# Kernel tuning notes

Hardware: AMD Instinct MI355X
Metric: run time of the kernel (lower is better)

The kernel has to match this reference:

```python
import jax, jax.numpy as jnp
import numpy as np

EPS = 1e-6
B, N, I, H, O, L = 8, 2048, 64, 128, 8, 3
K = O * L
ITERS, TAU, LAM, KNN = 3, 0.1, 0.5, 5

def _ln(x, g, b):
    m = x.mean(-1, keepdims=True)
    v = jnp.mean((x - m) ** 2, -1, keepdims=True)
    return (x - m) / jnp.sqrt(v + 1e-5) * g + b

def _gelu(x):
    return jax.nn.gelu(x, approximate=False)


def setup_inputs():
    ks = jax.random.split(jax.random.key(0), 16)
    rn = lambda k, sh, s=0.05: jax.random.normal(k, sh, jnp.float32) * s
    return {
        'x': jax.random.normal(ks[0], (B, N, I), jnp.float32),
        'enc_w1': rn(ks[1], (H, I)), 'enc_b1': jnp.zeros((H,), jnp.float32),
        'enc_g1': jnp.ones((H,), jnp.float32), 'enc_bb1': jnp.zeros((H,), jnp.float32),
        'enc_w2': rn(ks[2], (H, H)), 'enc_b2': jnp.zeros((H,), jnp.float32),
        'enc_g2': jnp.ones((H,), jnp.float32), 'enc_bb2': jnp.zeros((H,), jnp.float32),
        'sp_w1': rn(ks[3], (H, H + 1)), 'sp_b1': jnp.zeros((H,), jnp.float32),
        'sp_g': jnp.ones((H,), jnp.float32), 'sp_bb': jnp.zeros((H,), jnp.float32),
        'sp_w2': rn(ks[4], (1, H), 0.005), 'sp_b2': jnp.zeros((1,), jnp.float32),
        'object_space': rn(ks[5], (1, O, H), 0.1),
        'horizon_scale': jnp.float32(0.3),
        'level_times': jnp.array([1.0, 2.5, 4.0], jnp.float32),
        'base_horizons': jnp.array([0.9, 0.6, 0.3], jnp.float32),
        'gru_w_ih': rn(ks[6], (3 * H, H)), 'gru_w_hh': rn(ks[7], (3 * H, H)),
        'gru_b_ih': jnp.zeros((3 * H,), jnp.float32), 'gru_b_hh': jnp.zeros((3 * H,), jnp.float32),
        'mlp_w1': rn(ks[8], (H, H)), 'mlp_b1': jnp.zeros((H,), jnp.float32),
        'mlp_w2': rn(ks[9], (H, H)), 'mlp_b2': jnp.zeros((H,), jnp.float32),
        'norm_g': jnp.ones((H,), jnp.float32), 'norm_b': jnp.zeros((H,), jnp.float32),
    }


def reference(x, enc_w1, enc_b1, enc_g1, enc_bb1, enc_w2, enc_b2, enc_g2, enc_bb2, sp_w1, sp_b1, sp_g, sp_bb, sp_w2, sp_b2, object_space, horizon_scale, level_times, base_horizons, gru_w_ih, gru_w_hh, gru_b_ih, gru_b_hh, mlp_w1, mlp_b1, mlp_w2, mlp_b2, norm_g, norm_b):
    # feature encoder: Linear -> LN -> GELU -> Linear -> LN
    h = _gelu(_ln(x @ enc_w1.T + enc_b1, enc_g1, enc_bb1))
    spatial = _ln(h @ enc_w2.T + enc_b2, enc_g2, enc_bb2)  # (B,N,H)
    # local density via kNN mean distance (torch.cdist equivalent)
    sq = jnp.sum(x * x, -1)
    d2 = sq[:, :, None] + sq[:, None, :] - 2.0 * jnp.einsum('bnd,bmd->bnm', x, x)
    dist = jnp.sqrt(jnp.maximum(d2, 0.0))
    knn = -jax.lax.top_k(-dist, KNN + 1)[0]           # k+1 smallest, ascending
    density = jnp.tanh(knn[..., 1:].mean(-1))          # (B,N)
    # scale predictor: Linear -> LN -> GELU -> Linear -> Softplus
    s = jnp.concatenate([spatial, density[..., None]], -1)
    s = _gelu(_ln(s @ sp_w1.T + sp_b1, sp_g, sp_bb))
    pred_scale = jax.nn.softplus(s @ sp_w2.T + sp_b2)  # (B,N,1)
    pred_time = 5.0 - 1.5 * density[..., None] + 0.5 * pred_scale
    features = jnp.concatenate([pred_time, spatial], -1)  # (B,N,H+1)
    # scale-adaptive horizons, tiled object-major to match slot layout
    hz = jnp.clip(base_horizons[None, :, None] + (horizon_scale * (density - 0.5))[:, None, :], 0.1, 1.0)
    horizons = jnp.tile(hz, (1, O, 1))                 # (B,K,N)
    # worldlines
    obj = jnp.broadcast_to(object_space, (B, O, H))
    times = jnp.broadcast_to(jnp.tile(level_times, O)[None, :, None], (B, K, 1))
    slots = jnp.concatenate([times, jnp.repeat(obj, L, axis=1)], -1)  # (B,K,H+1)
    feats_sp = features[..., 1:]
    old_flat = obj.reshape(-1, H)
    attn = None
    for _ in range(ITERS):
        diff = features[:, None, :, :] - slots[:, :, None, :]  # (B,K,N,H+1)
        dt = diff[..., 0]
        dr2 = jnp.sum(diff[..., 1:] ** 2, -1)
        ls = dt * dt - dr2
        d_L = jnp.sign(ls) * jnp.sqrt(jnp.abs(ls) + EPS)
        r = jnp.sqrt(dr2)
        cone = horizons - r / (jnp.abs(dt) + EPS) - 10.0 * jax.nn.relu(-dt) - 5.0 * jax.nn.relu(r - jnp.abs(dt))
        logits = -jnp.abs(d_L) + LAM * jnp.tanh(cone)
        attn = jax.nn.softmax(logits / TAU, axis=1)      # softmax over slots
        w = attn / (attn.sum(2, keepdims=True) + 1e-8)
        upd = jnp.einsum('bkn,bnh->bkh', w, feats_sp)
        obj_upd = upd.reshape(B, O, L, H).sum(2).reshape(-1, H)
        # GRUCell (torch semantics)
        gi = obj_upd @ gru_w_ih.T + gru_b_ih
        gh = old_flat @ gru_w_hh.T + gru_b_hh
        gi_r, gi_z, gi_n = jnp.split(gi, 3, -1)
        gh_r, gh_z, gh_n = jnp.split(gh, 3, -1)
        rg = jax.nn.sigmoid(gi_r + gh_r)
        zg = jax.nn.sigmoid(gi_z + gh_z)
        ng = jnp.tanh(gi_n + rg * gh_n)
        new = ((1.0 - zg) * ng + zg * old_flat).reshape(B, O, H)
        t = _gelu(_ln(new, norm_g, norm_b) @ mlp_w1.T + mlp_b1) @ mlp_w2.T + mlp_b2
        new = new + 0.2 * t
        slots = jnp.concatenate([times, jnp.repeat(new, L, axis=1)], -1)
    return slots, attn, pred_time[..., 0], density
```

## Files before the change

kernel.cpp:

```cpp
#include <hip/hip_runtime.h>
#include <math.h>

constexpr int cB = 8, cN = 2048, cI = 64, cH = 128, cO = 8, cK = 24;
constexpr int ROWS = cB * cN;

constexpr size_t WS_SPATIAL = 0;
constexpr size_t WS_SQ      = WS_SPATIAL + (size_t)ROWS * cH;
constexpr size_t WS_GHS     = WS_SQ + ROWS;
constexpr size_t WS_NSQ0    = WS_GHS + (size_t)cO * 3 * cH;
constexpr size_t WS_NEWOBJ  = WS_NSQ0 + cO;
constexpr size_t WS_NSQ     = WS_NEWOBJ + (size_t)cB * cO * cH;
constexpr size_t WS_W1T     = WS_NSQ + (size_t)cB * cO;
constexpr size_t WS_W2T     = WS_W1T + 8192;
constexpr size_t WS_HW1T    = WS_W2T + 16384;
constexpr size_t WS_UPD3    = WS_HW1T + 16896;
constexpr size_t WS_S3      = WS_UPD3 + (size_t)3 * cB * cK * cH;
constexpr size_t WS_XBF     = WS_S3 + (size_t)3 * cB * cK;

constexpr size_t OUT_SLOTS = 0;
constexpr size_t OUT_ATTN  = (size_t)cB * cK * 129;
constexpr size_t OUT_PT    = OUT_ATTN + (size_t)cB * cK * cN;
constexpr size_t OUT_DEN   = OUT_PT + (size_t)cB * cN;

typedef __attribute__((ext_vector_type(8))) short bf16x8;
typedef __attribute__((ext_vector_type(4))) float f32x4;

__device__ __forceinline__ float gelu_f(float v){
  return 0.5f * v * (1.f + erff(v * 0.70710678118654752440f));
}
__device__ __forceinline__ short f2bf(float f){
  unsigned u = __float_as_uint(f);
  u += 0x7fffu + ((u >> 16) & 1u);
  return (short)(u >> 16);
}
__device__ __forceinline__ bf16x8 pack8(float4 a, float4 b){
  bf16x8 r;
  r[0]=f2bf(a.x); r[1]=f2bf(a.y); r[2]=f2bf(a.z); r[3]=f2bf(a.w);
  r[4]=f2bf(b.x); r[5]=f2bf(b.y); r[6]=f2bf(b.z); r[7]=f2bf(b.w);
  return r;
}
__device__ __forceinline__ float wred(float a){
  a += __shfl_xor(a, 1); a += __shfl_xor(a, 2); a += __shfl_xor(a, 4);
  a += __shfl_xor(a, 8); a += __shfl_xor(a, 16); a += __shfl_xor(a, 32);
  return a;
}

__global__ __launch_bounds__(256) void k_cvt_sq(const float* __restrict__ x, short* __restrict__ xbf,
                                                float* __restrict__ sq){
  int t = threadIdx.x;
  size_t base = (size_t)blockIdx.x * 2048;
  int r = t >> 3, e0 = (t & 7) * 8;
  const float4* xp = (const float4*)(x + base + (size_t)r * cI + e0);
  float4 v0 = xp[0], v1 = xp[1];
  *(bf16x8*)(xbf + base + (size_t)r * cI + e0) = pack8(v0, v1);
  float s = v0.x*v0.x + v0.y*v0.y + v0.z*v0.z + v0.w*v0.w
          + v1.x*v1.x + v1.y*v1.y + v1.z*v1.z + v1.w*v1.w;
  s += __shfl_xor(s, 1); s += __shfl_xor(s, 2); s += __shfl_xor(s, 4);
  if ((t & 7) == 0) sq[blockIdx.x * 32 + r] = s;
}

__global__ __launch_bounds__(256) void k_prep(const float* __restrict__ objsp, const float* __restrict__ w_hh,
                                              const float* __restrict__ b_hh,
                                              const float* __restrict__ ew1, const float* __restrict__ ew2,
                                              const float* __restrict__ spw1,
                                              float* __restrict__ ghs, float* __restrict__ nsq0,
                                              float* __restrict__ w1t, float* __restrict__ w2t,
                                              float* __restrict__ hw1t){
  int id = blockIdx.x * 256 + threadIdx.x;
  if (id < cO * 3 * cH){
    int o = id / (3 * cH), j = id % (3 * cH);
    const float* wr = w_hh + (size_t)j * cH;
    const float* ob = objsp + (size_t)o * cH;
    float a0=0,a1=0,a2=0,a3=0;
    #pragma unroll
    for (int h = 0; h < cH; h += 4){
      a0 += wr[h]*ob[h]; a1 += wr[h+1]*ob[h+1]; a2 += wr[h+2]*ob[h+2]; a3 += wr[h+3]*ob[h+3];
    }
    ghs[id] = (a0+a1)+(a2+a3) + b_hh[j];
  } else if (id < cO * 3 * cH + cO){
    int o = id - cO * 3 * cH;
    const float* ob = objsp + (size_t)o * cH;
    float s = 0.f;
    for (int h = 0; h < cH; ++h) s += ob[h]*ob[h];
    nsq0[o] = s;
  } else {
    int idx = id - (cO * 3 * cH + cO);
    if (idx < 8192){
      int dc = idx >> 9, rem = idx & 511, f = rem >> 2, j = rem & 3;
      w1t[idx] = ew1[f * cI + dc * 4 + j];
    } else if (idx < 24576){
      int k2 = idx - 8192;
      int dc = k2 >> 9, rem = k2 & 511, f = rem >> 2, j = rem & 3;
      w2t[k2] = ew2[f * cH + dc * 4 + j];
    } else if (idx < 41472){
      int k3 = idx - 24576;
      int dc = k3 >> 9, rem = k3 & 511, f = rem >> 2, j = rem & 3;
      int d = dc * 4 + j;
      hw1t[k3] = (d < 129) ? spw1[f * 129 + d] : 0.f;
    }
  }
}

__global__ __launch_bounds__(256) void k_pairwise(const short* __restrict__ xbf, const float* __restrict__ sq,
                                                  float* __restrict__ den_out){
  __shared__ float cand[4][16][101];
  int b  = blockIdx.x >> 7;
  int rt = blockIdx.x & 127;
  int r0 = rt * 16;
  int lane = threadIdx.x & 63, w = threadIdx.x >> 6;
  const short* xb = xbf + (size_t)b * cN * cI;

  int arow = r0 + (lane & 15);
  int koff = (lane >> 4) * 8;
  const bf16x8* ap = (const bf16x8*)(xb + (size_t)arow * cI + koff);
  bf16x8 a0 = ap[0];
  bf16x8 a1 = ap[4];

  float sqr[4];
  int rg0 = r0 + ((lane >> 4) << 2);
  #pragma unroll
  for (int j = 0; j < 4; ++j) sqr[j] = sq[b * cN + rg0 + j];

  float t6[4][6];
  #pragma unroll
  for (int j = 0; j < 4; ++j){
    #pragma unroll
    for (int q = 0; q < 6; ++q) t6[j][q] = 3e38f;
  }

  int cbase = w * 512;
  #pragma unroll 2
  for (int ct = 0; ct < 32; ++ct){
    int col0 = cbase + ct * 16;
    int brow = col0 + (lane & 15);
    const bf16x8* bp = (const bf16x8*)(xb + (size_t)brow * cI + koff);
    bf16x8 b0 = bp[0];
    bf16x8 b1 = bp[4];
    f32x4 acc = {0.f, 0.f, 0.f, 0.f};
    acc = __builtin_amdgcn_mfma_f32_16x16x32_bf16(a0, b0, acc, 0, 0, 0);
    acc = __builtin_amdgcn_mfma_f32_16x16x32_bf16(a1, b1, acc, 0, 0, 0);
    float sqc = sq[b * cN + col0 + (lane & 15)];
    #pragma unroll
    for (int j = 0; j < 4; ++j){
      float d2 = sqr[j] + sqc - 2.f * acc[j];
      d2 = fmaxf(d2, 0.f);
      if (d2 < t6[j][5]){
        if (d2 < t6[j][4]){ t6[j][5]=t6[j][4];
          if (d2 < t6[j][3]){ t6[j][4]=t6[j][3];
            if (d2 < t6[j][2]){ t6[j][3]=t6[j][2];
              if (d2 < t6[j][1]){ t6[j][2]=t6[j][1];
                if (d2 < t6[j][0]){ t6[j][1]=t6[j][0]; t6[j][0]=d2; } else t6[j][1]=d2;
              } else t6[j][2]=d2;
            } else t6[j][3]=d2;
          } else t6[j][4]=d2;
        } else t6[j][5]=d2;
      }
    }
  }
  int rloc = (lane >> 4) << 2;
  #pragma unroll
  for (int j = 0; j < 4; ++j){
    #pragma unroll
    for (int q = 0; q < 6; ++q) cand[w][rloc + j][(lane & 15) * 6 + q] = t6[j][q];
  }
  __syncthreads();
  int tt = threadIdx.x;
  if (tt < 64){
    int ww = tt >> 4, rr = tt & 15;
    const float* c = cand[ww][rr];
    float m0=3e38f,m1=3e38f,m2=3e38f,m3=3e38f,m4=3e38f,m5=3e38f;
    #pragma unroll
    for (int q = 0; q < 96; ++q){
      float v = c[q];
      if (v < m5){
        if (v<m4){ m5=m4; if (v<m3){ m4=m3; if (v<m2){ m3=m2; if (v<m1){ m2=m1; if (v<m0){ m1=m0; m0=v; } else m1=v; } else m2=v; } else m3=v; } else m4=v; } else m5=v;
      }
    }
    float* cw = cand[ww][rr];
    cw[0]=m0; cw[1]=m1; cw[2]=m2; cw[3]=m3; cw[4]=m4; cw[5]=m5;
  }
  __syncthreads();
  if (tt < 16){
    float m0=3e38f,m1=3e38f,m2=3e38f,m3=3e38f,m4=3e38f,m5=3e38f;
    #pragma unroll
    for (int ww = 0; ww < 4; ++ww){
      const float* c = cand[ww][tt];
      #pragma unroll
      for (int q = 0; q < 6; ++q){
        float v = c[q];
        if (v < m5){
          if (v<m4){ m5=m4; if (v<m3){ m4=m3; if (v<m2){ m3=m2; if (v<m1){ m2=m1; if (v<m0){ m1=m0; m0=v; } else m1=v; } else m2=v; } else m3=v; } else m4=v; } else m5=v;
        }
      }
    }
    float md = (sqrtf(m1)+sqrtf(m2)+sqrtf(m3)+sqrtf(m4)+sqrtf(m5)) * 0.2f;
    den_out[b * cN + r0 + tt] = tanhf(md);
  }
}

__global__ __launch_bounds__(256) void k_enc_head(const float* __restrict__ x, const float* __restrict__ den_in,
    const float* __restrict__ w1t, const float* __restrict__ b1v, const float* __restrict__ g1, const float* __restrict__ bb1,
    const float* __restrict__ w2t, const float* __restrict__ b2v, const float* __restrict__ g2, const float* __restrict__ bb2,
    const float* __restrict__ hw1t, const float* __restrict__ hb1, const float* __restrict__ hg, const float* __restrict__ hbb,
    const float* __restrict__ hw2, const float* __restrict__ hb2,
    float* __restrict__ spatial, float* __restrict__ pt_out){
  __shared__ __align__(16) float xbuf[16][68];
  __shared__ __align__(16) float hbuf[16][132];
  const int t = threadIdx.x, lane = t & 63, wid = t >> 6;
  const int row0 = blockIdx.x * 16;
  const int rbase = wid * 4;
  const int f0 = lane * 2;

  {
    const float4* xs = (const float4*)(x + (size_t)row0 * cI);
    float4 v = xs[t];
    *(float4*)&xbuf[t >> 4][(t & 15) * 4] = v;
  }
  if (t < 16){
    float dn = den_in[row0 + t];
    float* hd = &hbuf[t][128];
    hd[0] = dn; hd[1] = 0.f; hd[2] = 0.f; hd[3] = 0.f;
  }
  __syncthreads();

  float2 b1p  = *(const float2*)(b1v + f0);
  float2 g1p  = *(const float2*)(g1  + f0);
  float2 bb1p = *(const float2*)(bb1 + f0);
  float2 b2p  = *(const float2*)(b2v + f0);
  float2 g2p  = *(const float2*)(g2  + f0);
  float2 bb2p = *(const float2*)(bb2 + f0);
  float2 hb1p = *(const float2*)(hb1 + f0);
  float2 hgp  = *(const float2*)(hg  + f0);
  float2 hbbp = *(const float2*)(hbb + f0);
  float2 hw2p = *(const float2*)(hw2 + f0);

  float accA[4], accB[4];

  #pragma unroll
  for (int r = 0; r < 4; ++r){ accA[r] = b1p.x; accB[r] = b1p.y; }
  #pragma unroll 4
  for (int dc = 0; dc < 16; ++dc){
    float4 wA = *(const float4*)(w1t + ((size_t)dc * cH + f0) * 4);
    float4 wB = *(const float4*)(w1t + ((size_t)dc * cH + f0 + 1) * 4);
    #pragma unroll
    for (int r = 0; r < 4; ++r){
      float4 xv = *(const float4*)&xbuf[rbase + r][dc * 4];
      accA[r] += wA.x*xv.x + wA.y*xv.y + wA.z*xv.z + wA.w*xv.w;
      accB[r] += wB.x*xv.x + wB.y*xv.y + wB.z*xv.z + wB.w*xv.w;
    }
  }
  #pragma unroll
  for (int r = 0; r < 4; ++r){
    float sm = wred(accA[r] + accB[r]);
    float s2 = wred(accA[r]*accA[r] + accB[r]*accB[r]);
    float mean = sm * (1.f/128.f);
    float rstd = rsqrtf(s2 * (1.f/128.f) - mean*mean + 1e-5f);
    float hA = gelu_f((accA[r]-mean)*rstd*g1p.x + bb1p.x);
    float hB = gelu_f((accB[r]-mean)*rstd*g1p.y + bb1p.y);
    float2 hv = { hA, hB };
    *(float2*)&hbuf[rbase + r][f0] = hv;
  }
  __syncthreads();

  #pragma unroll
  for (int r = 0; r < 4; ++r){ accA[r] = b2p.x; accB[r] = b2p.y; }
  #pragma unroll 4
  for (int dc = 0; dc < 32; ++dc){
    float4 wA = *(const float4*)(w2t + ((size_t)dc * cH + f0) * 4);
    float4 wB = *(const float4*)(w2t + ((size_t)dc * cH + f0 + 1) * 4);
    #pragma unroll
    for (int r = 0; r < 4; ++r){
      float4 hv = *(const float4*)&hbuf[rbase + r][dc * 4];
      accA[r] += wA.x*hv.x + wA.y*hv.y + wA.z*hv.z + wA.w*hv.w;
      accB[r] += wB.x*hv.x + wB.y*hv.y + wB.z*hv.z + wB.w*hv.w;
    }
  }
  #pragma unroll
  for (int r = 0; r < 4; ++r){
    float sm = wred(accA[r] + accB[r]);
    float s2 = wred(accA[r]*accA[r] + accB[r]*accB[r]);
    float mean = sm * (1.f/128.f);
    float rstd = rsqrtf(s2 * (1.f/128.f) - mean*mean + 1e-5f);
    float sA = (accA[r]-mean)*rstd*g2p.x + bb2p.x;
    float sB = (accB[r]-mean)*rstd*g2p.y + bb2p.y;
    float2 sv = { sA, sB };
    *(float2*)(spatial + (size_t)(row0 + rbase + r) * cH + f0) = sv;
    *(float2*)&hbuf[rbase + r][f0] = sv;
  }
  __syncthreads();

  #pragma unroll
  for (int r = 0; r < 4; ++r){ accA[r] = hb1p.x; accB[r] = hb1p.y; }
  #pragma unroll 4
  for (int dc = 0; dc < 33; ++dc){
    float4 wA = *(const float4*)(hw1t + ((size_t)dc * cH + f0) * 4);
    float4 wB = *(const float4*)(hw1t + ((size_t)dc * cH + f0 + 1) * 4);
    #pragma unroll
    for (int r = 0; r < 4; ++r){
      float4 hv = *(const float4*)&hbuf[rbase + r][dc * 4];
      accA[r] += wA.x*hv.x + wA.y*hv.y + wA.z*hv.z + wA.w*hv.w;
      accB[r] += wB.x*hv.x + wB.y*hv.y + wB.z*hv.z + wB.w*hv.w;
    }
  }
  #pragma unroll
  for (int r = 0; r < 4; ++r){
    float sm = wred(accA[r] + accB[r]);
    float s2 = wred(accA[r]*accA[r] + accB[r]*accB[r]);
    float mean = sm * (1.f/128.f);
    float rstd = rsqrtf(s2 * (1.f/128.f) - mean*mean + 1e-5f);
    float e0 = gelu_f((accA[r]-mean)*rstd*hgp.x + hbbp.x);
    float e1 = gelu_f((accB[r]-mean)*rstd*hgp.y + hbbp.y);
    float part = wred(e0*hw2p.x + e1*hw2p.y);
    if (lane == r){
      float ps = part + hb2[0];
      float spl = fmaxf(ps, 0.f) + log1pf(expf(-fabsf(ps)));
      float dn = hbuf[rbase + r][128];
      pt_out[row0 + rbase + r] = 5.f - 1.5f*dn + 0.5f*spl;
    }
  }
}

__global__ __launch_bounds__(256) void k_attn_upd(const float* __restrict__ spatial, const float* __restrict__ pt_in,
    const float* __restrict__ den_in, const float* __restrict__ objp, int ob_stride,
    const float* __restrict__ nsqp, int nq_stride,
    const float* __restrict__ lt, const float* __restrict__ bh, const float* __restrict__ hs,
    float* __restrict__ attn_out, int writeAttn,
    float* __restrict__ upd_raw, float* __restrict__ Ssum){
  __shared__ float abuf[24][65];
  int blk = blockIdx.x;
  int b = blk >> 5, chunk = blk & 31;
  int n0 = chunk * 64;
  int t = threadIdx.x;
  int sub = t & 3, rl = t >> 2;
  int id = b * cN + n0 + rl;

  {
    float4 sv[8];
    const float4* sp4 = (const float4*)(spatial + (size_t)id * cH + sub * 32);
    #pragma unroll
    for (int i = 0; i < 8; ++i) sv[i] = sp4[i];
    float spn2 = 0.f;
    #pragma unroll
    for (int i = 0; i < 8; ++i) spn2 += sv[i].x*sv[i].x + sv[i].y*sv[i].y + sv[i].z*sv[i].z + sv[i].w*sv[i].w;

    const float* ob = objp + (size_t)b * ob_stride;
    float acc[8];
    #pragma unroll
    for (int o = 0; o < 8; ++o){
      const float4* orow = (const float4*)(ob + (size_t)o * cH + sub * 32);
      float a0=0,a1=0,a2=0,a3=0;
      #pragma unroll
      for (int i = 0; i < 8; ++i){ float4 w4 = orow[i];
        a0 += w4.x*sv[i].x; a1 += w4.y*sv[i].y; a2 += w4.z*sv[i].z; a3 += w4.w*sv[i].w; }
      acc[o] = (a0+a1)+(a2+a3);
    }
    spn2 += __shfl_xor(spn2, 1); spn2 += __shfl_xor(spn2, 2);
    #pragma unroll
    for (int o = 0; o < 8; ++o){ acc[o] += __shfl_xor(acc[o], 1); acc[o] += __shfl_xor(acc[o], 2); }

    if (sub == 0){
      const float* nq = nsqp + (size_t)b * nq_stride;
      float nsqv_[8];
      #pragma unroll
      for (int o = 0; o < 8; ++o) nsqv_[o] = nq[o];
      float pt = pt_in[id], den = den_in[id];
      float hsv = hs[0];
      float lts[3] = { lt[0], lt[1], lt[2] };
      float bhs[3] = { bh[0], bh[1], bh[2] };

      float logits[24];
      #pragma unroll
      for (int k = 0; k < 24; ++k){
        const int o = k / 3, l = k % 3;
        float dtv = pt - lts[l];
        float dr2 = fmaxf(spn2 + nsqv_[o] - 2.f * acc[o], 0.f);
        float ls  = dtv*dtv - dr2;
        float adL = sqrtf(fabsf(ls) + 1e-6f);
        float r   = sqrtf(dr2);
        float adt = fabsf(dtv);
        float hz  = fminf(fmaxf(bhs[l] + hsv * (den - 0.5f), 0.1f), 1.0f);
        float cone = hz - r / (adt + 1e-6f) - 10.f * fmaxf(-dtv, 0.f) - 5.f * fmaxf(r - adt, 0.f);
        logits[k] = (-adL + 0.5f * tanhf(cone)) * 10.f;
      }
      float mx = -3e38f;
      #pragma unroll
      for (int k = 0; k < 24; ++k) mx = fmaxf(mx, logits[k]);
      float es[24]; float ssum = 0.f;
      #pragma unroll
      for (int k = 0; k < 24; ++k){ es[k] = expf(logits[k] - mx); ssum += es[k]; }
      float inv = 1.f / ssum;
      #pragma unroll
      for (int k = 0; k < 24; ++k) abuf[k][rl] = es[k] * inv;
    }
  }
  __syncthreads();

  if (writeAttn){
    float* ao = attn_out + (size_t)b * cK * cN + n0;
    #pragma unroll
    for (int i = 0; i < 6; ++i){
      int idx = t + i * 256;
      ao[(size_t)(idx >> 6) * cN + (idx & 63)] = abuf[idx >> 6][idx & 63];
    }
  }

  int h = t & 127, g = t >> 7;
  float acc2[12];
  #pragma unroll
  for (int kk = 0; kk < 12; ++kk) acc2[kk] = 0.f;
  const float* sp = spatial + ((size_t)b * cN + n0) * cH + h;
  for (int ni = 0; ni < 64; ++ni){
    float spv = sp[(size_t)ni * cH];
    #pragma unroll
    for (int kk = 0; kk < 12; ++kk) acc2[kk] += abuf[g*12+kk][ni] * spv;
  }
  #pragma unroll
  for (int kk = 0; kk < 12; ++kk)
    atomicAdd(&upd_raw[((size_t)b * cK + g*12+kk) * cH + h], acc2[kk]);
  if (t < 24){
    float s = 0.f;
    #pragma unroll
    for (int j = 0; j < 64; ++j) s += abuf[t][j];
    atomicAdd(&Ssum[b * cK + t], s);
  }
}

__global__ __launch_bounds__(128) void k_gru(const float* __restrict__ upd_raw, const float* __restrict__ Ssum,
    const float* __restrict__ ghs, const float* __restrict__ objsp,
    const float* __restrict__ w_ih, const float* __restrict__ b_ih,
    const float* __restrict__ mw1, const float* __restrict__ mb1,
    const float* __restrict__ mw2, const float* __restrict__ mb2,
    const float* __restrict__ ng_, const float* __restrict__ nb_,
    const float* __restrict__ lt,
    float* __restrict__ newobj, float* __restrict__ nsq,
    float* __restrict__ slots_out, int writeSlots){
  __shared__ float ubuf[cH], lbuf[cH], gbuf[cH], red[8];
  int bo = blockIdx.x; int b = bo >> 3, o = bo & 7;
  int t = threadIdx.x;
  int lane = t & 63, wid = t >> 6;

  float u = 0.f;
  #pragma unroll
  for (int l = 0; l < 3; ++l){
    int k = o * 3 + l;
    float s = Ssum[b * cK + k] + 1e-8f;
    u += upd_raw[((size_t)b * cK + k) * cH + t] / s;
  }
  ubuf[t] = u;
  __syncthreads();

  float gi[3];
  #pragma unroll
  for (int j3 = 0; j3 < 3; ++j3){
    const float* wr = w_ih + ((size_t)j3 * cH + t) * cH;
    float a0=0,a1=0,a2=0,a3=0;
    #pragma unroll
    for (int d = 0; d < cH; d += 4){
      a0 += wr[d]*ubuf[d]; a1 += wr[d+1]*ubuf[d+1]; a2 += wr[d+2]*ubuf[d+2]; a3 += wr[d+3]*ubuf[d+3];
    }
    gi[j3] = (a0+a1)+(a2+a3) + b_ih[j3 * cH + t];
  }
  const float* gh = ghs + (size_t)o * 3 * cH;
  float ghr = gh[t], ghz = gh[cH + t], ghn = gh[2 * cH + t];
  float oldv = objsp[(size_t)o * cH + t];
  float rg = 1.f / (1.f + expf(-(gi[0] + ghr)));
  float zg = 1.f / (1.f + expf(-(gi[1] + ghz)));
  float ngv = tanhf(gi[2] + rg * ghn);
  float nv = (1.f - zg) * ngv + zg * oldv;

  float s1 = nv, s2 = nv * nv;
  #pragma unroll
  for (int m = 1; m < 64; m <<= 1){ s1 += __shfl_xor(s1, m); s2 += __shfl_xor(s2, m); }
  if (lane == 0){ red[wid] = s1; red[4 + wid] = s2; }
  __syncthreads();
  float mean = (red[0] + red[1]) * (1.f/128.f);
  float var  = (red[4] + red[5]) * (1.f/128.f) - mean * mean;
  float ln = (nv - mean) * rsqrtf(var + 1e-5f) * ng_[t] + nb_[t];
  lbuf[t] = ln;
  __syncthreads();

  const float* w1r = mw1 + (size_t)t * cH;
  {
    float a0=0,a1=0,a2=0,a3=0;
    #pragma unroll
    for (int d = 0; d < cH; d += 4){
      a0 += w1r[d]*lbuf[d]; a1 += w1r[d+1]*lbuf[d+1]; a2 += w1r[d+2]*lbuf[d+2]; a3 += w1r[d+3]*lbuf[d+3];
    }
    gbuf[t] = gelu_f((a0+a1)+(a2+a3) + mb1[t]);
  }
  __syncthreads();
  const float* w2r = mw2 + (size_t)t * cH;
  float m2v;
  {
    float a0=0,a1=0,a2=0,a3=0;
    #pragma unroll
    for (int d = 0; d < cH; d += 4){
      a0 += w2r[d]*gbuf[d]; a1 += w2r[d+1]*gbuf[d+1]; a2 += w2r[d+2]*gbuf[d+2]; a3 += w2r[d+3]*gbuf[d+3];
    }
    m2v = (a0+a1)+(a2+a3) + mb2[t];
  }
  float outv = nv + 0.2f * m2v;
  newobj[((size_t)b * cO + o) * cH + t] = outv;

  float qv = outv * outv;
  #pragma unroll
  for (int m = 1; m < 64; m <<= 1) qv += __shfl_xor(qv, m);
  __syncthreads();
  if (lane == 0) red[wid] = qv;
  __syncthreads();
  if (t == 0) nsq[b * cO + o] = red[0] + red[1];

  if (writeSlots){
    #pragma unroll
    for (int l = 0; l < 3; ++l){
      size_t base = ((size_t)b * cK + o * 3 + l) * 129;
      slots_out[base + 1 + t] = outv;
      if (t == 0) slots_out[base] = lt[l];
    }
  }
}

extern "C" void kernel_launch(void* const* d_in, const int* in_sizes, int n_in,
                              void* d_out, int out_size, void* d_ws, size_t ws_size,
                              hipStream_t stream){
  const float* x       = (const float*)d_in[0];
  const float* enc_w1  = (const float*)d_in[1];
  const float* enc_b1  = (const float*)d_in[2];
  const float* enc_g1  = (const float*)d_in[3];
  const float* enc_bb1 = (const float*)d_in[4];
  const float* enc_w2  = (const float*)d_in[5];
  const float* enc_b2  = (const float*)d_in[6];
  const float* enc_g2  = (const float*)d_in[7];
  const float* enc_bb2 = (const float*)d_in[8];
  const float* sp_w1   = (const float*)d_in[9];
  const float* sp_b1   = (const float*)d_in[10];
  const float* sp_g    = (const float*)d_in[11];
  const float* sp_bb   = (const float*)d_in[12];
  const float* sp_w2   = (const float*)d_in[13];
  const float* sp_b2   = (const float*)d_in[14];
  const float* objsp   = (const float*)d_in[15];
  const float* hscale  = (const float*)d_in[16];
  const float* ltimes  = (const float*)d_in[17];
  const float* bhor    = (const float*)d_in[18];
  const float* gw_ih   = (const float*)d_in[19];
  const float* gw_hh   = (const float*)d_in[20];
  const float* gb_ih   = (const float*)d_in[21];
  const float* gb_hh   = (const float*)d_in[22];
  const float* mw1     = (const float*)d_in[23];
  const float* mb1     = (const float*)d_in[24];
  const float* mw2     = (const float*)d_in[25];
  const float* mb2     = (const float*)d_in[26];
  const float* normg   = (const float*)d_in[27];
  const float* normb   = (const float*)d_in[28];
  (void)in_sizes; (void)n_in; (void)out_size; (void)ws_size;

  float* out = (float*)d_out;
  float* ws  = (float*)d_ws;

  float* spatial = ws + WS_SPATIAL;
  float* sq      = ws + WS_SQ;
  float* ghs     = ws + WS_GHS;
  float* nsq0    = ws + WS_NSQ0;
  float* newobj  = ws + WS_NEWOBJ;
  float* nsqv    = ws + WS_NSQ;
  float* w1t     = ws + WS_W1T;
  float* w2t     = ws + WS_W2T;
  float* hw1t    = ws + WS_HW1T;
  float* updr3   = ws + WS_UPD3;
  float* Ss3     = ws + WS_S3;
  short* xbf     = (short*)(ws + WS_XBF);

  hipMemsetAsync((void*)updr3, 0, (size_t)(3 * cB * cK * cH + 3 * cB * cK) * sizeof(float), stream);

  k_cvt_sq<<<dim3(ROWS / 32), dim3(256), 0, stream>>>(x, xbf, sq);
  k_prep<<<dim3(175), dim3(256), 0, stream>>>(objsp, gw_hh, gb_hh, enc_w1, enc_w2, sp_w1,
                                              ghs, nsq0, w1t, w2t, hw1t);
  k_pairwise<<<dim3(cB * (cN / 16)), dim3(256), 0, stream>>>(xbf, sq, out + OUT_DEN);
  k_enc_head<<<dim3(ROWS / 16), dim3(256), 0, stream>>>(x, out + OUT_DEN,
      w1t, enc_b1, enc_g1, enc_bb1, w2t, enc_b2, enc_g2, enc_bb2,
      hw1t, sp_b1, sp_g, sp_bb, sp_w2, sp_b2,
      spatial, out + OUT_PT);

  for (int it = 0; it < 3; ++it){
    float* updr = updr3 + (size_t)it * cB * cK * cH;
    float* Ss   = Ss3 + (size_t)it * cB * cK;
    const float* objp = (it == 0) ? objsp : newobj;
    int obst = (it == 0) ? 0 : cO * cH;
    const float* nqp = (it == 0) ? nsq0 : nsqv;
    int nqst = (it == 0) ? 0 : cO;
    k_attn_upd<<<dim3(cB * 32), dim3(256), 0, stream>>>(spatial, out + OUT_PT, out + OUT_DEN,
                                                        objp, obst, nqp, nqst,
                                                        ltimes, bhor, hscale,
                                                        out + OUT_ATTN, (it == 2) ? 1 : 0,
                                                        updr, Ss);
    k_gru<<<dim3(cB * cO), dim3(128), 0, stream>>>(updr, Ss, ghs, objsp, gw_ih, gb_ih,
                                                   mw1, mb1, mw2, mb2, normg, normb, ltimes,
                                                   newobj, nsqv, out + OUT_SLOTS, (it == 2) ? 1 : 0);
  }
}
```

Measured before the change: 340.5 us.

## Move encoder and spatial-head GEMMs to split-bf16 MFMA with pre-fragmented weights

Replaces the scalar FP32 dot-product loops in the encoder and spatial-head kernel with 16x16x32 bf16 MFMA instructions. Activations and weights are each split into hi and lo bf16 parts, and three MFMAs per tile approximate FP32 accuracy. The prep kernel now writes the weights in MFMA fragment order. Each wave handles 16 rows, with XOR-swizzled LDS buffers and per-wave layernorm reductions over 16 lanes. This cuts ALU time in the encoder but adds conversion work and some loss of precision from dropping the lo*lo term.

After: 315.0 us. 7.5% less time.

```diff
diff --git a/kernel.cpp b/kernel.cpp
--- a/kernel.cpp
+++ b/kernel.cpp
@@ -10,12 +10,17 @@
 constexpr size_t WS_NSQ0    = WS_GHS + (size_t)cO * 3 * cH;
 constexpr size_t WS_NEWOBJ  = WS_NSQ0 + cO;
 constexpr size_t WS_NSQ     = WS_NEWOBJ + (size_t)cB * cO * cH;
-constexpr size_t WS_W1T     = WS_NSQ + (size_t)cB * cO;
-constexpr size_t WS_W2T     = WS_W1T + 8192;
-constexpr size_t WS_HW1T    = WS_W2T + 16384;
-constexpr size_t WS_UPD3    = WS_HW1T + 16896;
+constexpr size_t WS_WFRAG   = WS_NSQ + (size_t)cB * cO;
+constexpr size_t WS_UPD3    = WS_WFRAG + 45056;
 constexpr size_t WS_S3      = WS_UPD3 + (size_t)3 * cB * cK * cH;
 constexpr size_t WS_XBF     = WS_S3 + (size_t)3 * cB * cK;
+
+constexpr size_t WF_W1H = 0;
+constexpr size_t WF_W1L = 8192;
+constexpr size_t WF_W2H = 16384;
+constexpr size_t WF_W2L = 32768;
+constexpr size_t WF_WHH = 49152;
+constexpr size_t WF_WHL = 69632;
 
 constexpr size_t OUT_SLOTS = 0;
 constexpr size_t OUT_ATTN  = (size_t)cB * cK * 129;
@@ -32,6 +37,9 @@
   unsigned u = __float_as_uint(f);
   u += 0x7fffu + ((u >> 16) & 1u);
   return (short)(u >> 16);
+}
+__device__ __forceinline__ float bf2f(short h){
+  return __uint_as_float(((unsigned)(unsigned short)h) << 16);
 }
 __device__ __forceinline__ bf16x8 pack8(float4 a, float4 b){
   bf16x8 r;
@@ -39,10 +47,23 @@
   r[4]=f2bf(b.x); r[5]=f2bf(b.y); r[6]=f2bf(b.z); r[7]=f2bf(b.w);
   return r;
 }
-__device__ __forceinline__ float wred(float a){
-  a += __shfl_xor(a, 1); a += __shfl_xor(a, 2); a += __shfl_xor(a, 4);
-  a += __shfl_xor(a, 8); a += __shfl_xor(a, 16); a += __shfl_xor(a, 32);
+__device__ __forceinline__ float qred16(float a){
+  a += __shfl_xor(a, 1); a += __shfl_xor(a, 2); a += __shfl_xor(a, 4); a += __shfl_xor(a, 8);
   return a;
+}
+__device__ __forceinline__ void load_split_frag(const float* buf, int off, bf16x8& hi, bf16x8& lo){
+  float4 u0 = *(const float4*)&buf[off];
+  float4 u1 = *(const float4*)&buf[off + 4];
+  float v[8] = {u0.x,u0.y,u0.z,u0.w,u1.x,u1.y,u1.z,u1.w};
+  #pragma unroll
+  for (int i = 0; i < 8; ++i){
+    short h = f2bf(v[i]);
+    hi[i] = h;
+    lo[i] = f2bf(v[i] - bf2f(h));
+  }
+}
+__device__ __forceinline__ int lidx(int row, int col, int stride){
+  return row * stride + (col ^ ((row & 3) << 3));
 }
 
 __global__ __launch_bounds__(256) void k_cvt_sq(const float* __restrict__ x, short* __restrict__ xbf,
@@ -64,8 +85,7 @@
                                               const float* __restrict__ ew1, const float* __restrict__ ew2,
                                               const float* __restrict__ spw1,
                                               float* __restrict__ ghs, float* __restrict__ nsq0,
-                                              float* __restrict__ w1t, float* __restrict__ w2t,
-                                              float* __restrict__ hw1t){
+                                              short* __restrict__ wf){
   int id = blockIdx.x * 256 + threadIdx.x;
   if (id < cO * 3 * cH){
     int o = id / (3 * cH), j = id % (3 * cH);
@@ -85,19 +105,34 @@
     nsq0[o] = s;
   } else {
     int idx = id - (cO * 3 * cH + cO);
+    if (idx >= 45056) return;
+    float w; size_t hoff, loff;
+    int e, nc;
     if (idx < 8192){
-      int dc = idx >> 9, rem = idx & 511, f = rem >> 2, j = rem & 3;
-      w1t[idx] = ew1[f * cI + dc * 4 + j];
+      e = idx; nc = 2;
+      int i = e & 7, l = (e >> 3) & 63, r = e >> 9;
+      int c = r % nc, ft = r / nc;
+      int f = ft * 16 + (l & 15), k = c * 32 + (l >> 4) * 8 + i;
+      w = ew1[f * cI + k];
+      hoff = WF_W1H + e; loff = WF_W1L + e;
     } else if (idx < 24576){
-      int k2 = idx - 8192;
-      int dc = k2 >> 9, rem = k2 & 511, f = rem >> 2, j = rem & 3;
-      w2t[k2] = ew2[f * cH + dc * 4 + j];
-    } else if (idx < 41472){
-      int k3 = idx - 24576;
-      int dc = k3 >> 9, rem = k3 & 511, f = rem >> 2, j = rem & 3;
-      int d = dc * 4 + j;
-      hw1t[k3] = (d < 129) ? spw1[f * 129 + d] : 0.f;
-    }
+      e = idx - 8192; nc = 4;
+      int i = e & 7, l = (e >> 3) & 63, r = e >> 9;
+      int c = r % nc, ft = r / nc;
+      int f = ft * 16 + (l & 15), k = c * 32 + (l >> 4) * 8 + i;
+      w = ew2[f * cH + k];
+      hoff = WF_W2H + e; loff = WF_W2L + e;
+    } else {
+      e = idx - 24576; nc = 5;
+      int i = e & 7, l = (e >> 3) & 63, r = e >> 9;
+      int c = r % nc, ft = r / nc;
+      int f = ft * 16 + (l & 15), k = c * 32 + (l >> 4) * 8 + i;
+      w = (k < 129) ? spw1[f * 129 + k] : 0.f;
+      hoff = WF_WHH + e; loff = WF_WHL + e;
+    }
+    short h = f2bf(w);
+    wf[hoff] = h;
+    wf[loff] = f2bf(w - bf2f(h));
   }
 }
 
@@ -198,124 +233,197 @@
   }
 }
 
-__global__ __launch_bounds__(256) void k_enc_head(const float* __restrict__ x, const float* __restrict__ den_in,
-    const float* __restrict__ w1t, const float* __restrict__ b1v, const float* __restrict__ g1, const float* __restrict__ bb1,
-    const float* __restrict__ w2t, const float* __restrict__ b2v, const float* __restrict__ g2, const float* __restrict__ bb2,
-    const float* __restrict__ hw1t, const float* __restrict__ hb1, const float* __restrict__ hg, const float* __restrict__ hbb,
+__global__ __launch_bounds__(128) void k_enc_head(const float* __restrict__ x, const float* __restrict__ den_in,
+    const short* __restrict__ wf,
+    const float* __restrict__ b1, const float* __restrict__ g1, const float* __restrict__ bb1,
+    const float* __restrict__ b2, const float* __restrict__ g2, const float* __restrict__ bb2,
+    const float* __restrict__ hb1, const float* __restrict__ hg, const float* __restrict__ hbb,
     const float* __restrict__ hw2, const float* __restrict__ hb2,
     float* __restrict__ spatial, float* __restrict__ pt_out){
-  __shared__ __align__(16) float xbuf[16][68];
-  __shared__ __align__(16) float hbuf[16][132];
-  const int t = threadIdx.x, lane = t & 63, wid = t >> 6;
-  const int row0 = blockIdx.x * 16;
-  const int rbase = wid * 4;
-  const int f0 = lane * 2;
+  __shared__ __align__(16) float xs_[2][16 * 68];
+  __shared__ __align__(16) float hs_[2][16 * 164];
+  const int t = threadIdx.x, lane = t & 63, wv = t >> 6;
+  const int row0 = blockIdx.x * 32 + wv * 16;
+  float* xbuf = xs_[wv];
+  float* hbuf = hs_[wv];
+  const int r15 = lane & 15, q = lane >> 4;
+  const int qx = (q ^ (r15 & 3)) << 3;
 
   {
-    const float4* xs = (const float4*)(x + (size_t)row0 * cI);
-    float4 v = xs[t];
-    *(float4*)&xbuf[t >> 4][(t & 15) * 4] = v;
-  }
-  if (t < 16){
-    float dn = den_in[row0 + t];
-    float* hd = &hbuf[t][128];
-    hd[0] = dn; hd[1] = 0.f; hd[2] = 0.f; hd[3] = 0.f;
-  }
-  __syncthreads();
-
-  float2 b1p  = *(const float2*)(b1v + f0);
-  float2 g1p  = *(const float2*)(g1  + f0);
-  float2 bb1p = *(const float2*)(bb1 + f0);
-  float2 b2p  = *(const float2*)(b2v + f0);
-  float2 g2p  = *(const float2*)(g2  + f0);
-  float2 bb2p = *(const float2*)(bb2 + f0);
-  float2 hb1p = *(const float2*)(hb1 + f0);
-  float2 hgp  = *(const float2*)(hg  + f0);
-  float2 hbbp = *(const float2*)(hbb + f0);
-  float2 hw2p = *(const float2*)(hw2 + f0);
-
-  float accA[4], accB[4];
-
-  #pragma unroll
-  for (int r = 0; r < 4; ++r){ accA[r] = b1p.x; accB[r] = b1p.y; }
-  #pragma unroll 4
-  for (int dc = 0; dc < 16; ++dc){
-    float4 wA = *(const float4*)(w1t + ((size_t)dc * cH + f0) * 4);
-    float4 wB = *(const float4*)(w1t + ((size_t)dc * cH + f0 + 1) * 4);
-    #pragma unroll
-    for (int r = 0; r < 4; ++r){
-      float4 xv = *(const float4*)&xbuf[rbase + r][dc * 4];
-      accA[r] += wA.x*xv.x + wA.y*xv.y + wA.z*xv.z + wA.w*xv.w;
-      accB[r] += wB.x*xv.x + wB.y*xv.y + wB.z*xv.z + wB.w*xv.w;
-    }
-  }
-  #pragma unroll
-  for (int r = 0; r < 4; ++r){
-    float sm = wred(accA[r] + accB[r]);
-    float s2 = wred(accA[r]*accA[r] + accB[r]*accB[r]);
-    float mean = sm * (1.f/128.f);
-    float rstd = rsqrtf(s2 * (1.f/128.f) - mean*mean + 1e-5f);
-    float hA = gelu_f((accA[r]-mean)*rstd*g1p.x + bb1p.x);
-    float hB = gelu_f((accB[r]-mean)*rstd*g1p.y + bb1p.y);
-    float2 hv = { hA, hB };
-    *(float2*)&hbuf[rbase + r][f0] = hv;
-  }
-  __syncthreads();
-
-  #pragma unroll
-  for (int r = 0; r < 4; ++r){ accA[r] = b2p.x; accB[r] = b2p.y; }
-  #pragma unroll 4
-  for (int dc = 0; dc < 32; ++dc){
-    float4 wA = *(const float4*)(w2t + ((size_t)dc * cH + f0) * 4);
-    float4 wB = *(const float4*)(w2t + ((size_t)dc * cH + f0 + 1) * 4);
-    #pragma unroll
-    for (int r = 0; r < 4; ++r){
-      float4 hv = *(const float4*)&hbuf[rbase + r][dc * 4];
-      accA[r] += wA.x*hv.x + wA.y*hv.y + wA.z*hv.z + wA.w*hv.w;
-      accB[r] += wB.x*hv.x + wB.y*hv.y + wB.z*hv.z + wB.w*hv.w;
-    }
-  }
-  #pragma unroll
-  for (int r = 0; r < 4; ++r){
-    float sm = wred(accA[r] + accB[r]);
-    float s2 = wred(accA[r]*accA[r] + accB[r]*accB[r]);
-    float mean = sm * (1.f/128.f);
-    float rstd = rsqrtf(s2 * (1.f/128.f) - mean*mean + 1e-5f);
-    float sA = (accA[r]-mean)*rstd*g2p.x + bb2p.x;
-    float sB = (accB[r]-mean)*rstd*g2p.y + bb2p.y;
-    float2 sv = { sA, sB };
-    *(float2*)(spatial + (size_t)(row0 + rbase + r) * cH + f0) = sv;
-    *(float2*)&hbuf[rbase + r][f0] = sv;
-  }
-  __syncthreads();
-
-  #pragma unroll
-  for (int r = 0; r < 4; ++r){ accA[r] = hb1p.x; accB[r] = hb1p.y; }
-  #pragma unroll 4
-  for (int dc = 0; dc < 33; ++dc){
-    float4 wA = *(const float4*)(hw1t + ((size_t)dc * cH + f0) * 4);
-    float4 wB = *(const float4*)(hw1t + ((size_t)dc * cH + f0 + 1) * 4);
-    #pragma unroll
-    for (int r = 0; r < 4; ++r){
-      float4 hv = *(const float4*)&hbuf[rbase + r][dc * 4];
-      accA[r] += wA.x*hv.x + wA.y*hv.y + wA.z*hv.z + wA.w*hv.w;
-      accB[r] += wB.x*hv.x + wB.y*hv.y + wB.z*hv.z + wB.w*hv.w;
-    }
-  }
-  #pragma unroll
-  for (int r = 0; r < 4; ++r){
-    float sm = wred(accA[r] + accB[r]);
-    float s2 = wred(accA[r]*accA[r] + accB[r]*accB[r]);
-    float mean = sm * (1.f/128.f);
-    float rstd = rsqrtf(s2 * (1.f/128.f) - mean*mean + 1e-5f);
-    float e0 = gelu_f((accA[r]-mean)*rstd*hgp.x + hbbp.x);
-    float e1 = gelu_f((accB[r]-mean)*rstd*hgp.y + hbbp.y);
-    float part = wred(e0*hw2p.x + e1*hw2p.y);
-    if (lane == r){
-      float ps = part + hb2[0];
-      float spl = fmaxf(ps, 0.f) + log1pf(expf(-fabsf(ps)));
-      float dn = hbuf[rbase + r][128];
-      pt_out[row0 + rbase + r] = 5.f - 1.5f*dn + 0.5f*spl;
+    const float4* xg = (const float4*)(x + (size_t)row0 * cI);
+    #pragma unroll
+    for (int k = 0; k < 4; ++k){
+      int f4 = k * 64 + lane;
+      int row = f4 >> 4, c4 = (f4 & 15) * 4;
+      float4 v = xg[f4];
+      *(float4*)&xbuf[lidx(row, c4, 68)] = v;
+    }
+  }
+  __syncthreads();
+
+  f32x4 acc[8];
+  const short* w1h = wf + WF_W1H; const short* w1l = wf + WF_W1L;
+  const short* w2h = wf + WF_W2H; const short* w2l = wf + WF_W2L;
+  const short* whh = wf + WF_WHH; const short* whl = wf + WF_WHL;
+
+  #pragma unroll
+  for (int ft = 0; ft < 8; ++ft) acc[ft] = (f32x4){0.f,0.f,0.f,0.f};
+  #pragma unroll
+  for (int c = 0; c < 2; ++c){
+    bf16x8 ah, al;
+    load_split_frag(xbuf, r15 * 68 + c * 32 + qx, ah, al);
+    #pragma unroll
+    for (int ft = 0; ft < 8; ++ft){
+      bf16x8 bh = *(const bf16x8*)&w1h[(size_t)(((ft*2 + c)*64) + lane) * 8];
+      bf16x8 bl = *(const bf16x8*)&w1l[(size_t)(((ft*2 + c)*64) + lane) * 8];
+      acc[ft] = __builtin_amdgcn_mfma_f32_16x16x32_bf16(al, bh, acc[ft], 0, 0, 0);
+      acc[ft] = __builtin_amdgcn_mfma_f32_16x16x32_bf16(ah, bl, acc[ft], 0, 0, 0);
+      acc[ft] = __builtin_amdgcn_mfma_f32_16x16x32_bf16(ah, bh, acc[ft], 0, 0, 0);
+    }
+  }
+  {
+    float sm0=0,sm1=0,sm2=0,sm3=0, s20=0,s21=0,s22=0,s23=0;
+    #pragma unroll
+    for (int ft = 0; ft < 8; ++ft){
+      float bv = b1[ft*16 + r15];
+      float v0 = acc[ft][0]+bv, v1 = acc[ft][1]+bv, v2 = acc[ft][2]+bv, v3 = acc[ft][3]+bv;
+      acc[ft][0]=v0; acc[ft][1]=v1; acc[ft][2]=v2; acc[ft][3]=v3;
+      sm0+=v0; sm1+=v1; sm2+=v2; sm3+=v3;
+      s20+=v0*v0; s21+=v1*v1; s22+=v2*v2; s23+=v3*v3;
+    }
+    sm0=qred16(sm0); sm1=qred16(sm1); sm2=qred16(sm2); sm3=qred16(sm3);
+    s20=qred16(s20); s21=qred16(s21); s22=qred16(s22); s23=qred16(s23);
+    float mean[4] = { sm0*(1.f/128.f), sm1*(1.f/128.f), sm2*(1.f/128.f), sm3*(1.f/128.f) };
+    float rstd[4] = { rsqrtf(s20*(1.f/128.f)-mean[0]*mean[0]+1e-5f),
+                      rsqrtf(s21*(1.f/128.f)-mean[1]*mean[1]+1e-5f),
+                      rsqrtf(s22*(1.f/128.f)-mean[2]*mean[2]+1e-5f),
+                      rsqrtf(s23*(1.f/128.f)-mean[3]*mean[3]+1e-5f) };
+    #pragma unroll
+    for (int ft = 0; ft < 8; ++ft){
+      float gv = g1[ft*16 + r15], bbv = bb1[ft*16 + r15];
+      #pragma unroll
+      for (int j = 0; j < 4; ++j){
+        float e = gelu_f((acc[ft][j]-mean[j])*rstd[j]*gv + bbv);
+        hbuf[lidx(q*4 + j, ft*16 + r15, 164)] = e;
+      }
+    }
+  }
+  __syncthreads();
+
+  #pragma unroll
+  for (int ft = 0; ft < 8; ++ft) acc[ft] = (f32x4){0.f,0.f,0.f,0.f};
+  #pragma unroll
+  for (int c = 0; c < 4; ++c){
+    bf16x8 ah, al;
+    load_split_frag(hbuf, r15 * 164 + c * 32 + qx, ah, al);
+    #pragma unroll
+    for (int ft = 0; ft < 8; ++ft){
+      bf16x8 bh = *(const bf16x8*)&w2h[(size_t)(((ft*4 + c)*64) + lane) * 8];
+      bf16x8 bl = *(const bf16x8*)&w2l[(size_t)(((ft*4 + c)*64) + lane) * 8];
+      acc[ft] = __builtin_amdgcn_mfma_f32_16x16x32_bf16(al, bh, acc[ft], 0, 0, 0);
+      acc[ft] = __builtin_amdgcn_mfma_f32_16x16x32_bf16(ah, bl, acc[ft], 0, 0, 0);
+      acc[ft] = __builtin_amdgcn_mfma_f32_16x16x32_bf16(ah, bh, acc[ft], 0, 0, 0);
+    }
+  }
+  __syncthreads();
+  {
+    float sm0=0,sm1=0,sm2=0,sm3=0, s20=0,s21=0,s22=0,s23=0;
+    #pragma unroll
+    for (int ft = 0; ft < 8; ++ft){
+      float bv = b2[ft*16 + r15];
+      float v0 = acc[ft][0]+bv, v1 = acc[ft][1]+bv, v2 = acc[ft][2]+bv, v3 = acc[ft][3]+bv;
+      acc[ft][0]=v0; acc[ft][1]=v1; acc[ft][2]=v2; acc[ft][3]=v3;
+      sm0+=v0; sm1+=v1; sm2+=v2; sm3+=v3;
+      s20+=v0*v0; s21+=v1*v1; s22+=v2*v2; s23+=v3*v3;
+    }
+    sm0=qred16(sm0); sm1=qred16(sm1); sm2=qred16(sm2); sm3=qred16(sm3);
+    s20=qred16(s20); s21=qred16(s21); s22=qred16(s22); s23=qred16(s23);
+    float mean[4] = { sm0*(1.f/128.f), sm1*(1.f/128.f), sm2*(1.f/128.f), sm3*(1.f/128.f) };
+    float rstd[4] = { rsqrtf(s20*(1.f/128.f)-mean[0]*mean[0]+1e-5f),
+                      rsqrtf(s21*(1.f/128.f)-mean[1]*mean[1]+1e-5f),
+                      rsqrtf(s22*(1.f/128.f)-mean[2]*mean[2]+1e-5f),
+                      rsqrtf(s23*(1.f/128.f)-mean[3]*mean[3]+1e-5f) };
+    #pragma unroll
+    for (int ft = 0; ft < 8; ++ft){
+      float gv = g2[ft*16 + r15], bbv = bb2[ft*16 + r15];
+      #pragma unroll
+      for (int j = 0; j < 4; ++j){
+        float s = (acc[ft][j]-mean[j])*rstd[j]*gv + bbv;
+        hbuf[lidx(q*4 + j, ft*16 + r15, 164)] = s;
+      }
+    }
+    #pragma unroll
+    for (int i = 0; i < 8; ++i){
+      int flat = lane * 8 + i;
+      int row = flat >> 5, col = 128 + (flat & 31);
+      float v = ((flat & 31) == 0) ? den_in[row0 + row] : 0.f;
+      hbuf[lidx(row, col, 164)] = v;
+    }
+  }
+  __syncthreads();
+
+  {
+    #pragma unroll
+    for (int k = 0; k < 8; ++k){
+      int f4 = k * 64 + lane;
+      int row = f4 >> 5, c4 = (f4 & 31) * 4;
+      float4 v = *(const float4*)&hbuf[lidx(row, c4, 164)];
+      *(float4*)(spatial + (size_t)(row0 + row) * cH + c4) = v;
+    }
+  }
+
+  #pragma unroll
+  for (int ft = 0; ft < 8; ++ft) acc[ft] = (f32x4){0.f,0.f,0.f,0.f};
+  #pragma unroll
+  for (int c = 0; c < 5; ++c){
+    bf16x8 ah, al;
+    load_split_frag(hbuf, r15 * 164 + c * 32 + qx, ah, al);
+    #pragma unroll
+    for (int ft = 0; ft < 8; ++ft){
+      bf16x8 bh = *(const bf16x8*)&whh[(size_t)(((ft*5 + c)*64) + lane) * 8];
+      bf16x8 bl = *(const bf16x8*)&whl[(size_t)(((ft*5 + c)*64) + lane) * 8];
+      acc[ft] = __builtin_amdgcn_mfma_f32_16x16x32_bf16(al, bh, acc[ft], 0, 0, 0);
+      acc[ft] = __builtin_amdgcn_mfma_f32_16x16x32_bf16(ah, bl, acc[ft], 0, 0, 0);
+      acc[ft] = __builtin_amdgcn_mfma_f32_16x16x32_bf16(ah, bh, acc[ft], 0, 0, 0);
+    }
+  }
+  {
+    float sm0=0,sm1=0,sm2=0,sm3=0, s20=0,s21=0,s22=0,s23=0;
+    #pragma unroll
+    for (int ft = 0; ft < 8; ++ft){
+      float bv = hb1[ft*16 + r15];
+      float v0 = acc[ft][0]+bv, v1 = acc[ft][1]+bv, v2 = acc[ft][2]+bv, v3 = acc[ft][3]+bv;
+      acc[ft][0]=v0; acc[ft][1]=v1; acc[ft][2]=v2; acc[ft][3]=v3;
+      sm0+=v0; sm1+=v1; sm2+=v2; sm3+=v3;
+      s20+=v0*v0; s21+=v1*v1; s22+=v2*v2; s23+=v3*v3;
+    }
+    sm0=qred16(sm0); sm1=qred16(sm1); sm2=qred16(sm2); sm3=qred16(sm3);
+    s20=qred16(s20); s21=qred16(s21); s22=qred16(s22); s23=qred16(s23);
+    float mean[4] = { sm0*(1.f/128.f), sm1*(1.f/128.f), sm2*(1.f/128.f), sm3*(1.f/128.f) };
+    float rstd[4] = { rsqrtf(s20*(1.f/128.f)-mean[0]*mean[0]+1e-5f),
+                      rsqrtf(s21*(1.f/128.f)-mean[1]*mean[1]+1e-5f),
+                      rsqrtf(s22*(1.f/128.f)-mean[2]*mean[2]+1e-5f),
+                      rsqrtf(s23*(1.f/128.f)-mean[3]*mean[3]+1e-5f) };
+    float part0=0, part1=0, part2=0, part3=0;
+    #pragma unroll
+    for (int ft = 0; ft < 8; ++ft){
+      float gv = hg[ft*16 + r15], bbv = hbb[ft*16 + r15], w2v = hw2[ft*16 + r15];
+      part0 += gelu_f((acc[ft][0]-mean[0])*rstd[0]*gv + bbv) * w2v;
+      part1 += gelu_f((acc[ft][1]-mean[1])*rstd[1]*gv + bbv) * w2v;
+      part2 += gelu_f((acc[ft][2]-mean[2])*rstd[2]*gv + bbv) * w2v;
+      part3 += gelu_f((acc[ft][3]-mean[3])*rstd[3]*gv + bbv) * w2v;
+    }
+    part0=qred16(part0); part1=qred16(part1); part2=qred16(part2); part3=qred16(part3);
+    float parts[4] = { part0, part1, part2, part3 };
+    #pragma unroll
+    for (int j = 0; j < 4; ++j){
+      if (r15 == j){
+        int row = q * 4 + j;
+        float ps = parts[j] + hb2[0];
+        float spl = fmaxf(ps, 0.f) + log1pf(expf(-fabsf(ps)));
+        float dn = den_in[row0 + row];
+        pt_out[row0 + row] = 5.f - 1.5f*dn + 0.5f*spl;
+      }
     }
   }
 }
@@ -563,9 +671,7 @@
   float* nsq0    = ws + WS_NSQ0;
   float* newobj  = ws + WS_NEWOBJ;
   float* nsqv    = ws + WS_NSQ;
-  float* w1t     = ws + WS_W1T;
-  float* w2t     = ws + WS_W2T;
-  float* hw1t    = ws + WS_HW1T;
+  short* wf      = (short*)(ws + WS_WFRAG);
   float* updr3   = ws + WS_UPD3;
   float* Ss3     = ws + WS_S3;
   short* xbf     = (short*)(ws + WS_XBF);
@@ -573,12 +679,12 @@
   hipMemsetAsync((void*)updr3, 0, (size_t)(3 * cB * cK * cH + 3 * cB * cK) * sizeof(float), stream);
 
   k_cvt_sq<<<dim3(ROWS / 32), dim3(256), 0, stream>>>(x, xbf, sq);
-  k_prep<<<dim3(175), dim3(256), 0, stream>>>(objsp, gw_hh, gb_hh, enc_w1, enc_w2, sp_w1,
-                                              ghs, nsq0, w1t, w2t, hw1t);
+  k_prep<<<dim3(189), dim3(256), 0, stream>>>(objsp, gw_hh, gb_hh, enc_w1, enc_w2, sp_w1,
+                                              ghs, nsq0, wf);
   k_pairwise<<<dim3(cB * (cN / 16)), dim3(256), 0, stream>>>(xbf, sq, out + OUT_DEN);
-  k_enc_head<<<dim3(ROWS / 16), dim3(256), 0, stream>>>(x, out + OUT_DEN,
-      w1t, enc_b1, enc_g1, enc_bb1, w2t, enc_b2, enc_g2, enc_bb2,
-      hw1t, sp_b1, sp_g, sp_bb, sp_w2, sp_b2,
+  k_enc_head<<<dim3(ROWS / 32), dim3(128), 0, stream>>>(x, out + OUT_DEN, wf,
+      enc_b1, enc_g1, enc_bb1, enc_b2, enc_g2, enc_bb2,
+      sp_b1, sp_g, sp_bb, sp_w2, sp_b2,
       spatial, out + OUT_PT);
 
   for (int it = 0; it < 3; ++it){
```
